# Kernel optimization log

Measured on AMD Instinct MI355X. Metric: run time of the kernel, lower is better.

The kernel has to match this reference:

```python
import jax, jax.numpy as jnp
import numpy as np

N_NODES = 100000
N_EDGES = 1600000
DIMS = [512, 200, 175, 125, 75, 50]


def setup_inputs() -> dict:
    key = jax.random.key(0)
    ks = jax.random.split(key, 12)
    inp = {
        "x": jax.random.normal(ks[0], (N_NODES, DIMS[0]), dtype=jnp.float32),
        "edge_index": jax.random.randint(ks[1], (2, N_EDGES), 0, N_NODES, dtype=jnp.int32),
    }
    for i in range(5):
        fan_in, fan_out = DIMS[i], DIMS[i + 1]
        scale = 1.0 / np.sqrt(fan_in)
        inp[f"W{i+1}"] = jax.random.uniform(ks[2 + 2 * i], (fan_in, fan_out), minval=-scale, maxval=scale, dtype=jnp.float32)
        inp[f"b{i+1}"] = jnp.zeros((fan_out,), dtype=jnp.float32)
    return inp


def _gcn_norm(edge_index, n_nodes):
    # add self loops, then symmetric normalization D^-1/2 (A+I) D^-1/2
    loop = jnp.arange(n_nodes, dtype=edge_index.dtype)
    src = jnp.concatenate([edge_index[0], loop])
    dst = jnp.concatenate([edge_index[1], loop])
    deg = jax.ops.segment_sum(jnp.ones_like(dst, dtype=jnp.float32), dst, num_segments=n_nodes)
    dinv = jnp.where(deg > 0, jax.lax.rsqrt(deg), 0.0)
    norm = dinv[src] * dinv[dst]  # [E+N]
    return src, dst, norm


def _gcn_layer(x, W, b, src, dst, norm, n_nodes):
    h = x @ W                                   # [N, out] dense GEMM
    msg = h[src] * norm[:, None]                # gather + scale  [E+N, out]
    agg = jax.ops.segment_sum(msg, dst, num_segments=n_nodes)  # scatter-add
    return agg + b


def reference(x, edge_index, W1, b1, W2, b2, W3, b3, W4, b4, W5, b5):
    n = x.shape[0]
    src, dst, norm = _gcn_norm(edge_index, n)
    h = jax.nn.relu(_gcn_layer(x, W1, b1, src, dst, norm, n))
    h = jax.nn.relu(_gcn_layer(h, W2, b2, src, dst, norm, n))
    h = jax.nn.relu(_gcn_layer(h, W3, b3, src, dst, norm, n))
    h = jax.nn.relu(_gcn_layer(h, W4, b4, src, dst, norm, n))
    return _gcn_layer(h, W5, b5, src, dst, norm, n)
```

## Files before the change

kernel.cpp:

```cpp
#include <hip/hip_runtime.h>
#include <hip/hip_bf16.h>


typedef float f32x4 __attribute__((ext_vector_type(4)));
typedef short bf16x8 __attribute__((ext_vector_type(8)));
typedef ushort u16x4 __attribute__((ext_vector_type(4)));
typedef ushort u16x8 __attribute__((ext_vector_type(8)));

static const int GDIMS[6] = {512, 200, 175, 125, 75, 50};


__global__ void zero_kernel(int* __restrict__ p, int n) {
    int i = blockIdx.x * blockDim.x + threadIdx.x;
    for (; i < n; i += gridDim.x * blockDim.x) p[i] = 0;
}

__global__ void hist_kernel(const int* __restrict__ dst, int E, int* __restrict__ deg) {
    int i = blockIdx.x * blockDim.x + threadIdx.x;
    for (; i < E; i += gridDim.x * blockDim.x) atomicAdd(&deg[dst[i]], 1);
}

__global__ __launch_bounds__(1024) void scan_kernel(const int* __restrict__ deg,
                                                    int* __restrict__ rowptr, int N) {
    __shared__ int sums[1024];
    int t = threadIdx.x;
    int chunk = (N + 1023) >> 10;
    int lo = t * chunk;
    int hi = lo + chunk; if (hi > N) hi = N;
    if (lo > N) lo = N;
    int s = 0;
    for (int i = lo; i < hi; ++i) s += deg[i];
    sums[t] = s;
    __syncthreads();
    for (int off = 1; off < 1024; off <<= 1) {
        int v = (t >= off) ? sums[t - off] : 0;
        __syncthreads();
        sums[t] += v;
        __syncthreads();
    }
    int run = (t > 0) ? sums[t - 1] : 0;
    for (int i = lo; i < hi; ++i) { rowptr[i] = run; run += deg[i]; }
    if (t == 1023) rowptr[N] = run;
}

__global__ void dinv_kernel(const int* __restrict__ deg, float* __restrict__ dinv, int N) {
    int i = blockIdx.x * blockDim.x + threadIdx.x;
    for (; i < N; i += gridDim.x * blockDim.x)
        dinv[i] = rsqrtf((float)(deg[i] + 1));
}

__global__ void copy_kernel(const int* __restrict__ a, int* __restrict__ b, int n) {
    int i = blockIdx.x * blockDim.x + threadIdx.x;
    for (; i < n; i += gridDim.x * blockDim.x) b[i] = a[i];
}

__global__ void scatter_kernel(const int* __restrict__ src, const int* __restrict__ dst,
                               int E, int* __restrict__ cursor, int* __restrict__ csrc) {
    int i = blockIdx.x * blockDim.x + threadIdx.x;
    for (; i < E; i += gridDim.x * blockDim.x) {
        int d = dst[i];
        int pos = atomicAdd(&cursor[d], 1);
        csrc[pos] = src[i];
    }
}


__global__ void wsplit_kernel(const float* __restrict__ W, int K, int Nout,
                              int Kp, ushort* __restrict__ Whi, ushort* __restrict__ Wlo) {
    int k = blockIdx.x * blockDim.x + threadIdx.x;
    int n = blockIdx.y;
    if (k >= Kp) return;
    float v = (k < K && n < Nout) ? W[(size_t)k * Nout + n] : 0.f;
    __bf16 h = (__bf16)v;
    ushort hb = __builtin_bit_cast(ushort, h);
    float hf = __builtin_bit_cast(float, (unsigned)hb << 16);
    __bf16 l = (__bf16)(v - hf);
    Whi[(size_t)n * Kp + k] = hb;
    Wlo[(size_t)n * Kp + k] = __builtin_bit_cast(ushort, l);
}


__device__ inline f32x4 mfma16(bf16x8 a, bf16x8 b, f32x4 c) {
    return __builtin_amdgcn_mfma_f32_16x16x32_bf16(a, b, c, 0, 0, 0);
}

__device__ inline void split8(f32x4 a0, f32x4 a1, u16x8& hi, u16x8& lo) {
    float af[8] = {a0[0], a0[1], a0[2], a0[3], a1[0], a1[1], a1[2], a1[3]};
#pragma unroll
    for (int e = 0; e < 8; ++e) {
        __bf16 h = (__bf16)af[e];
        ushort hb = __builtin_bit_cast(ushort, h);
        float hf = __builtin_bit_cast(float, (unsigned)hb << 16);
        __bf16 l = (__bf16)(af[e] - hf);
        hi[e] = hb;
        lo[e] = __builtin_bit_cast(ushort, l);
    }
}


template<int WM, int WN>
__global__ __launch_bounds__(WM * WN * 64) void gemm_t(
    const float* __restrict__ A, int lda, int Arows,
    const ushort* __restrict__ Bhi, const ushort* __restrict__ Blo, int Kp,
    const float* __restrict__ dinv, int N,
    float* __restrict__ C, int ldc)
{
    constexpr int BM = WM * 64;
    constexpr int T = WM * WN * 64;
    constexpr int SROW = BM + 2;
    __shared__ ushort Ah[4 * SROW * 8];
    __shared__ ushort Al[4 * SROW * 8];

    const int tid = threadIdx.x;
    const int lane = tid & 63;
    const int wave = tid >> 6;
    const int wm = (WM == 1) ? 0 : (wave % WM);
    const int wn = (WM == 1) ? wave : (wave / WM);
    const int m0 = blockIdx.x * BM;
    const int kg = lane >> 4;
    const int l16 = lane & 15;

    const ushort* bp[4];
#pragma unroll
    for (int fn = 0; fn < 4; ++fn) {
        int n = wn * 64 + fn * 16 + l16;
        bp[fn] = Bhi + (size_t)n * Kp + kg * 8;
    }
    const size_t lo_off = (size_t)(Blo - Bhi);

    f32x4 acc[4][4];
#pragma unroll
    for (int i = 0; i < 4; ++i)
#pragma unroll
        for (int j = 0; j < 4; ++j) acc[i][j] = (f32x4)0.f;

    for (int k0 = 0; k0 < Kp; k0 += 32) {
        for (int j = tid; j < BM * 4; j += T) {
            int row = j >> 2, jk = j & 3;
            int gr = m0 + row; if (gr > Arows - 1) gr = Arows - 1;
            const float* ap = A + (size_t)gr * lda + k0 + jk * 8;
            f32x4 a0 = *(const f32x4*)ap;
            f32x4 a1 = *(const f32x4*)(ap + 4);
            u16x8 hi, lo;
            split8(a0, a1, hi, lo);
            int idx = (jk * SROW + row) * 8;
            *(u16x8*)&Ah[idx] = hi;
            *(u16x8*)&Al[idx] = lo;
        }
        __syncthreads();
        bf16x8 bh[4], bl[4], ah[4], al[4];
#pragma unroll
        for (int fn = 0; fn < 4; ++fn) {
            bh[fn] = *(const bf16x8*)(bp[fn] + k0);
            bl[fn] = *(const bf16x8*)(bp[fn] + lo_off + k0);
        }
#pragma unroll
        for (int fm = 0; fm < 4; ++fm) {
            int idx = (kg * SROW + wm * 64 + fm * 16 + l16) * 8;
            ah[fm] = *(const bf16x8*)&Ah[idx];
            al[fm] = *(const bf16x8*)&Al[idx];
        }
#pragma unroll
        for (int fm = 0; fm < 4; ++fm)
#pragma unroll
            for (int fn = 0; fn < 4; ++fn) {
                acc[fm][fn] = mfma16(ah[fm], bh[fn], acc[fm][fn]);
                acc[fm][fn] = mfma16(ah[fm], bl[fn], acc[fm][fn]);
                acc[fm][fn] = mfma16(al[fm], bh[fn], acc[fm][fn]);
            }
        __syncthreads();
    }

#pragma unroll
    for (int fm = 0; fm < 4; ++fm)
#pragma unroll
        for (int fn = 0; fn < 4; ++fn) {
            int col = wn * 64 + fn * 16 + l16;
            if (col < ldc) {
#pragma unroll
                for (int r = 0; r < 4; ++r) {
                    int row = m0 + wm * 64 + fm * 16 + kg * 4 + r;
                    float dv = (row < N) ? dinv[row] : 0.f;
                    C[(size_t)row * ldc + col] = acc[fm][fn][r] * dv;
                }
            }
        }
}


template<int WM, int WN>
__global__ __launch_bounds__(WM * WN * 64) void gemm_ps(
    const ushort* __restrict__ Ahi, const ushort* __restrict__ Alo, int lda, int Arows,
    const ushort* __restrict__ Bhi, const ushort* __restrict__ Blo, int Kp,
    const float* __restrict__ dinv, int N,
    float* __restrict__ C, int ldc)
{
    constexpr int BM = WM * 64;
    constexpr int T = WM * WN * 64;
    constexpr int SROW = BM + 2;
    __shared__ ushort Ah[4 * SROW * 8];
    __shared__ ushort Al[4 * SROW * 8];

    const int tid = threadIdx.x;
    const int lane = tid & 63;
    const int wave = tid >> 6;
    const int wm = (WM == 1) ? 0 : (wave % WM);
    const int wn = (WM == 1) ? wave : (wave / WM);
    const int m0 = blockIdx.x * BM;
    const int kg = lane >> 4;
    const int l16 = lane & 15;

    const size_t alo = (size_t)(Alo - Ahi);
    const ushort* bp[4];
#pragma unroll
    for (int fn = 0; fn < 4; ++fn) {
        int n = wn * 64 + fn * 16 + l16;
        bp[fn] = Bhi + (size_t)n * Kp + kg * 8;
    }
    const size_t blo = (size_t)(Blo - Bhi);

    f32x4 acc[4][4];
#pragma unroll
    for (int i = 0; i < 4; ++i)
#pragma unroll
        for (int j = 0; j < 4; ++j) acc[i][j] = (f32x4)0.f;

    for (int k0 = 0; k0 < Kp; k0 += 32) {
        for (int j = tid; j < BM * 4; j += T) {
            int row = j >> 2, jk = j & 3;
            int gr = m0 + row; if (gr > Arows - 1) gr = Arows - 1;
            const ushort* s = Ahi + (size_t)gr * lda + k0 + jk * 8;
            int idx = (jk * SROW + row) * 8;
            *(u16x8*)&Ah[idx] = *(const u16x8*)s;
            *(u16x8*)&Al[idx] = *(const u16x8*)(s + alo);
        }
        __syncthreads();
        bf16x8 bh[4], bl[4], ah[4], al[4];
#pragma unroll
        for (int fn = 0; fn < 4; ++fn) {
            bh[fn] = *(const bf16x8*)(bp[fn] + k0);
            bl[fn] = *(const bf16x8*)(bp[fn] + blo + k0);
        }
#pragma unroll
        for (int fm = 0; fm < 4; ++fm) {
            int idx = (kg * SROW + wm * 64 + fm * 16 + l16) * 8;
            ah[fm] = *(const bf16x8*)&Ah[idx];
            al[fm] = *(const bf16x8*)&Al[idx];
        }
#pragma unroll
        for (int fm = 0; fm < 4; ++fm)
#pragma unroll
            for (int fn = 0; fn < 4; ++fn) {
                acc[fm][fn] = mfma16(ah[fm], bh[fn], acc[fm][fn]);
                acc[fm][fn] = mfma16(ah[fm], bl[fn], acc[fm][fn]);
                acc[fm][fn] = mfma16(al[fm], bh[fn], acc[fm][fn]);
            }
        __syncthreads();
    }

#pragma unroll
    for (int fm = 0; fm < 4; ++fm)
#pragma unroll
        for (int fn = 0; fn < 4; ++fn) {
            int col = wn * 64 + fn * 16 + l16;
            if (col < ldc) {
#pragma unroll
                for (int r = 0; r < 4; ++r) {
                    int row = m0 + wm * 64 + fm * 16 + kg * 4 + r;
                    float dv = (row < N) ? dinv[row] : 0.f;
                    C[(size_t)row * ldc + col] = acc[fm][fn][r] * dv;
                }
            }
        }
}


template<int ND4T, bool FIN>
__global__ __launch_bounds__(256) void agg_t(
    const float* __restrict__ g, int ld4,
    const int* __restrict__ rowptr, const int* __restrict__ csrc,
    const float* __restrict__ dinv, const float* __restrict__ bias,
    int D, int N,
    ushort* __restrict__ Ahi, ushort* __restrict__ Alo, int ldo,
    float* __restrict__ outF, int ldof)
{
    unsigned gt = blockIdx.x * 256u + threadIdx.x;
    unsigned node = gt / (unsigned)ND4T;
    unsigned f4 = gt - node * (unsigned)ND4T;
    if (node >= (unsigned)N) return;

    const f32x4* g4 = (const f32x4*)g;
    const unsigned l4 = (unsigned)ld4;

    f32x4 a0 = g4[(size_t)node * l4 + f4];
    f32x4 a1 = (f32x4)0.f, a2 = (f32x4)0.f, a3 = (f32x4)0.f;
    int beg = rowptr[node], end = rowptr[node + 1];
    int j = beg;
    for (; j + 3 < end; j += 4) {
        unsigned s0 = csrc[j], s1 = csrc[j + 1], s2 = csrc[j + 2], s3 = csrc[j + 3];
        a0 += g4[(size_t)s0 * l4 + f4];
        a1 += g4[(size_t)s1 * l4 + f4];
        a2 += g4[(size_t)s2 * l4 + f4];
        a3 += g4[(size_t)s3 * l4 + f4];
    }
    for (; j < end; ++j) a0 += g4[(size_t)csrc[j] * l4 + f4];

    f32x4 s = (a0 + a1) + (a2 + a3);
    float di = dinv[node];

    if (FIN) {
#pragma unroll
        for (int e = 0; e < 4; ++e) {
            int f = (int)f4 * 4 + e;
            if (f < D) outF[(size_t)node * ldof + f] = fmaf(di, s[e], bias[f]);
        }
    } else {
        u16x4 hv, lv;
#pragma unroll
        for (int e = 0; e < 4; ++e) {
            int f = (int)f4 * 4 + e;
            float val = 0.f;
            if (f < D) val = fmaxf(fmaf(di, s[e], bias[f]), 0.f);
            __bf16 h = (__bf16)val;
            ushort hb = __builtin_bit_cast(ushort, h);
            float hf = __builtin_bit_cast(float, (unsigned)hb << 16);
            __bf16 l = (__bf16)(val - hf);
            hv[e] = hb;
            lv[e] = __builtin_bit_cast(ushort, l);
        }
        *(u16x4*)(Ahi + (size_t)node * ldo + f4 * 4) = hv;
        *(u16x4*)(Alo + (size_t)node * ldo + f4 * 4) = lv;
    }
}


extern "C" void kernel_launch(void* const* d_in, const int* in_sizes, int n_in,
                              void* d_out, int out_size, void* d_ws, size_t ws_size,
                              hipStream_t stream) {
    const float* x = (const float*)d_in[0];
    const int* ei = (const int*)d_in[1];
    int E = in_sizes[1] / 2;
    int N = in_sizes[0] / GDIMS[0];
    int Mp = ((N + 255) / 256) * 256;
    const int* src = ei;
    const int* dst = ei + E;

    const float* W[5];
    const float* bia[5];
    for (int i = 0; i < 5; ++i) {
        W[i] = (const float*)d_in[2 + 2 * i];
        bia[i] = (const float*)d_in[3 + 2 * i];
    }

    char* ws = (char*)d_ws;
    size_t off = 0;
    auto alloc = [&](size_t bytes) -> void* {
        void* p = ws + off;
        off += (bytes + 255) & ~(size_t)255;
        return p;
    };
    int* deg = (int*)alloc((size_t)N * 4);
    int* rowptr = (int*)alloc((size_t)(N + 1) * 4);
    int* cursor = (int*)alloc((size_t)N * 4);
    float* dinv = (float*)alloc((size_t)N * 4);
    int* csrc = (int*)alloc((size_t)E * 4);
    float* g = (float*)alloc((size_t)Mp * 224 * 4);
    ushort* Ahi = (ushort*)alloc((size_t)Mp * 224 * 2);
    ushort* Alo = (ushort*)alloc((size_t)Mp * 224 * 2);
    ushort* Whi[5];
    ushort* Wlo[5];
    int NB[5] = {256, 192, 128, 128, 64};
    int KP[5] = {512, 224, 192, 128, 96};
    for (int l = 0; l < 5; ++l) {
        Whi[l] = (ushort*)alloc((size_t)NB[l] * KP[l] * 2);
        Wlo[l] = (ushort*)alloc((size_t)NB[l] * KP[l] * 2);
    }
    (void)ws_size;

    zero_kernel<<<1024, 256, 0, stream>>>(deg, N);
    hist_kernel<<<2048, 256, 0, stream>>>(dst, E, deg);
    scan_kernel<<<1, 1024, 0, stream>>>(deg, rowptr, N);
    dinv_kernel<<<512, 256, 0, stream>>>(deg, dinv, N);
    copy_kernel<<<512, 256, 0, stream>>>(rowptr, cursor, N);
    scatter_kernel<<<2048, 256, 0, stream>>>(src, dst, E, cursor, csrc);

    for (int l = 0; l < 5; ++l) {
        dim3 gw((KP[l] + 255) / 256, NB[l]);
        wsplit_kernel<<<gw, 256, 0, stream>>>(W[l], GDIMS[l], GDIMS[l + 1], KP[l],
                                              Whi[l], Wlo[l]);
    }

    auto aggBlocks = [&](int nd4t) { return (unsigned)(((size_t)N * nd4t + 255) / 256); };

    gemm_t<1, 4><<<Mp / 64, 256, 0, stream>>>(x, 512, N, Whi[0], Wlo[0], 512,
                                              dinv, N, g, 224);
    agg_t<56, false><<<aggBlocks(56), 256, 0, stream>>>(g, 56, rowptr, csrc, dinv,
                                                        bia[0], 200, N, Ahi, Alo, 224,
                                                        nullptr, 0);
    gemm_ps<1, 3><<<Mp / 64, 192, 0, stream>>>(Ahi, Alo, 224, N, Whi[1], Wlo[1], 224,
                                               dinv, N, g, 192);
    agg_t<48, false><<<aggBlocks(48), 256, 0, stream>>>(g, 48, rowptr, csrc, dinv,
                                                        bia[1], 175, N, Ahi, Alo, 192,
                                                        nullptr, 0);
    gemm_ps<2, 2><<<Mp / 128, 256, 0, stream>>>(Ahi, Alo, 192, N, Whi[2], Wlo[2], 192,
                                                dinv, N, g, 128);
    agg_t<32, false><<<aggBlocks(32), 256, 0, stream>>>(g, 32, rowptr, csrc, dinv,
                                                        bia[2], 125, N, Ahi, Alo, 128,
                                                        nullptr, 0);
    gemm_ps<2, 2><<<Mp / 128, 256, 0, stream>>>(Ahi, Alo, 128, N, Whi[3], Wlo[3], 128,
                                                dinv, N, g, 96);
    agg_t<24, false><<<aggBlocks(24), 256, 0, stream>>>(g, 24, rowptr, csrc, dinv,
                                                        bia[3], 75, N, Ahi, Alo, 96,
                                                        nullptr, 0);
    gemm_ps<4, 1><<<Mp / 256, 256, 0, stream>>>(Ahi, Alo, 96, N, Whi[4], Wlo[4], 96,
                                                dinv, N, g, 64);
    agg_t<13, true><<<aggBlocks(13), 256, 0, stream>>>(g, 16, rowptr, csrc, dinv,
                                                       bia[4], 50, N, nullptr, nullptr, 0,
                                                       (float*)d_out, 50);
    (void)out_size; (void)n_in;
}
```

Baseline: 1.376 ms.

## Pre-swizzle activations and weights into MFMA fragment layout, drop LDS staging

The aggregation kernels now write the bf16 hi/lo activations straight into a blocked layout that matches the 16x16x32 MFMA fragments. The weight-splitting kernel writes the weights for layers 2-5 in the same layout. The new GEMM then loads A and B fragments directly from global memory, with no shared-memory staging and no barriers. Aggregation also switches to a power-of-two number of lanes per node, which leaves some lanes idle and stops writing zeros to the padded feature columns, so those columns may keep stale data.

```diff
diff --git a/kernel.cpp b/kernel.cpp
--- a/kernel.cpp
+++ b/kernel.cpp
@@ -79,6 +79,24 @@
     Wlo[(size_t)n * Kp + k] = __builtin_bit_cast(ushort, l);
 }
 
+__global__ void wsplit_sw(const float* __restrict__ W, int K, int Nout,
+                          int Kp, ushort* __restrict__ Whi, ushort* __restrict__ Wlo) {
+    int k = blockIdx.x * blockDim.x + threadIdx.x;
+    int n = blockIdx.y;
+    if (k >= Kp) return;
+    int KQ = Kp >> 3;
+    float v = (k < K && n < Nout) ? W[(size_t)k * Nout + n] : 0.f;
+    __bf16 h = (__bf16)v;
+    ushort hb = __builtin_bit_cast(ushort, h);
+    float hf = __builtin_bit_cast(float, (unsigned)hb << 16);
+    __bf16 l = (__bf16)(v - hf);
+    int mb = n >> 6, fm = (n >> 4) & 3, l16 = n & 15;
+    int kq = k >> 3, ko = k & 7;
+    size_t idx = ((((size_t)mb * KQ + kq) * 4 + fm) * 16 + l16) * 8 + ko;
+    Whi[idx] = hb;
+    Wlo[idx] = __builtin_bit_cast(ushort, l);
+}
+
 
 __device__ inline f32x4 mfma16(bf16x8 a, bf16x8 b, f32x4 c) {
     return __builtin_amdgcn_mfma_f32_16x16x32_bf16(a, b, c, 0, 0, 0);
@@ -188,36 +206,30 @@
 }
 
 
-template<int WM, int WN>
-__global__ __launch_bounds__(WM * WN * 64) void gemm_ps(
-    const ushort* __restrict__ Ahi, const ushort* __restrict__ Alo, int lda, int Arows,
-    const ushort* __restrict__ Bhi, const ushort* __restrict__ Blo, int Kp,
+template<int WN>
+__global__ __launch_bounds__(WN * 64) void gemm_sw(
+    const ushort* __restrict__ Ahi, const ushort* __restrict__ Alo, int KQ, int Kp,
+    const ushort* __restrict__ Bhi, const ushort* __restrict__ Blo,
     const float* __restrict__ dinv, int N,
     float* __restrict__ C, int ldc)
 {
-    constexpr int BM = WM * 64;
-    constexpr int T = WM * WN * 64;
-    constexpr int SROW = BM + 2;
-    __shared__ ushort Ah[4 * SROW * 8];
-    __shared__ ushort Al[4 * SROW * 8];
-
-    const int tid = threadIdx.x;
-    const int lane = tid & 63;
-    const int wave = tid >> 6;
-    const int wm = (WM == 1) ? 0 : (wave % WM);
-    const int wn = (WM == 1) ? wave : (wave / WM);
-    const int m0 = blockIdx.x * BM;
+    const int lane = threadIdx.x & 63;
+    const int wn = threadIdx.x >> 6;
+    const int m0 = blockIdx.x * 64;
+    const int mb = m0 >> 6;
     const int kg = lane >> 4;
     const int l16 = lane & 15;
 
     const size_t alo = (size_t)(Alo - Ahi);
+    const size_t blo = (size_t)(Blo - Bhi);
+    const ushort* ap[4];
     const ushort* bp[4];
 #pragma unroll
-    for (int fn = 0; fn < 4; ++fn) {
-        int n = wn * 64 + fn * 16 + l16;
-        bp[fn] = Bhi + (size_t)n * Kp + kg * 8;
-    }
-    const size_t blo = (size_t)(Blo - Bhi);
+    for (int fm = 0; fm < 4; ++fm)
+        ap[fm] = Ahi + ((((size_t)mb * KQ + kg) * 4 + fm) * 16 + l16) * 8;
+#pragma unroll
+    for (int fn = 0; fn < 4; ++fn)
+        bp[fn] = Bhi + ((((size_t)wn * KQ + kg) * 4 + fn) * 16 + l16) * 8;
 
     f32x4 acc[4][4];
 #pragma unroll
@@ -225,27 +237,19 @@
 #pragma unroll
         for (int j = 0; j < 4; ++j) acc[i][j] = (f32x4)0.f;
 
-    for (int k0 = 0; k0 < Kp; k0 += 32) {
-        for (int j = tid; j < BM * 4; j += T) {
-            int row = j >> 2, jk = j & 3;
-            int gr = m0 + row; if (gr > Arows - 1) gr = Arows - 1;
-            const ushort* s = Ahi + (size_t)gr * lda + k0 + jk * 8;
-            int idx = (jk * SROW + row) * 8;
-            *(u16x8*)&Ah[idx] = *(const u16x8*)s;
-            *(u16x8*)&Al[idx] = *(const u16x8*)(s + alo);
-        }
-        __syncthreads();
-        bf16x8 bh[4], bl[4], ah[4], al[4];
+    const int nsteps = Kp >> 5;
+    for (int t = 0; t < nsteps; ++t) {
+        const size_t off = (size_t)t * 2048;
+        bf16x8 ah[4], al4[4], bh[4], bl[4];
+#pragma unroll
+        for (int fm = 0; fm < 4; ++fm) {
+            ah[fm] = *(const bf16x8*)(ap[fm] + off);
+            al4[fm] = *(const bf16x8*)(ap[fm] + alo + off);
+        }
 #pragma unroll
         for (int fn = 0; fn < 4; ++fn) {
-            bh[fn] = *(const bf16x8*)(bp[fn] + k0);
-            bl[fn] = *(const bf16x8*)(bp[fn] + blo + k0);
-        }
-#pragma unroll
-        for (int fm = 0; fm < 4; ++fm) {
-            int idx = (kg * SROW + wm * 64 + fm * 16 + l16) * 8;
-            ah[fm] = *(const bf16x8*)&Ah[idx];
-            al[fm] = *(const bf16x8*)&Al[idx];
+            bh[fn] = *(const bf16x8*)(bp[fn] + off);
+            bl[fn] = *(const bf16x8*)(bp[fn] + blo + off);
         }
 #pragma unroll
         for (int fm = 0; fm < 4; ++fm)
@@ -253,9 +257,8 @@
             for (int fn = 0; fn < 4; ++fn) {
                 acc[fm][fn] = mfma16(ah[fm], bh[fn], acc[fm][fn]);
                 acc[fm][fn] = mfma16(ah[fm], bl[fn], acc[fm][fn]);
-                acc[fm][fn] = mfma16(al[fm], bh[fn], acc[fm][fn]);
+                acc[fm][fn] = mfma16(al4[fm], bh[fn], acc[fm][fn]);
             }
-        __syncthreads();
     }
 
 #pragma unroll
@@ -266,7 +269,7 @@
             if (col < ldc) {
 #pragma unroll
                 for (int r = 0; r < 4; ++r) {
-                    int row = m0 + wm * 64 + fm * 16 + kg * 4 + r;
+                    int row = m0 + fm * 16 + kg * 4 + r;
                     float dv = (row < N) ? dinv[row] : 0.f;
                     C[(size_t)row * ldc + col] = acc[fm][fn][r] * dv;
                 }
@@ -275,50 +278,49 @@
 }
 
 
-template<int ND4T, bool FIN>
-__global__ __launch_bounds__(256) void agg_t(
-    const float* __restrict__ g, int ld4,
+template<int L>
+__global__ __launch_bounds__(256) void agg_sw(
+    const float* __restrict__ g, int ldg, int nd4,
     const int* __restrict__ rowptr, const int* __restrict__ csrc,
     const float* __restrict__ dinv, const float* __restrict__ bias,
     int D, int N,
-    ushort* __restrict__ Ahi, ushort* __restrict__ Alo, int ldo,
-    float* __restrict__ outF, int ldof)
+    ushort* __restrict__ Ahi, ushort* __restrict__ Alo, int KQ,
+    float* __restrict__ outF, int ldof, int fin)
 {
-    unsigned gt = blockIdx.x * 256u + threadIdx.x;
-    unsigned node = gt / (unsigned)ND4T;
-    unsigned f4 = gt - node * (unsigned)ND4T;
-    if (node >= (unsigned)N) return;
+    int node = blockIdx.x * (256 / L) + threadIdx.x / L;
+    if (node >= N) return;
+    int f4 = threadIdx.x & (L - 1);
+    if (f4 >= nd4) return;
 
     const f32x4* g4 = (const f32x4*)g;
-    const unsigned l4 = (unsigned)ld4;
-
-    f32x4 a0 = g4[(size_t)node * l4 + f4];
+    int ld4 = ldg >> 2;
+    f32x4 a0 = g4[(size_t)node * ld4 + f4];
     f32x4 a1 = (f32x4)0.f, a2 = (f32x4)0.f, a3 = (f32x4)0.f;
     int beg = rowptr[node], end = rowptr[node + 1];
     int j = beg;
     for (; j + 3 < end; j += 4) {
-        unsigned s0 = csrc[j], s1 = csrc[j + 1], s2 = csrc[j + 2], s3 = csrc[j + 3];
-        a0 += g4[(size_t)s0 * l4 + f4];
-        a1 += g4[(size_t)s1 * l4 + f4];
-        a2 += g4[(size_t)s2 * l4 + f4];
-        a3 += g4[(size_t)s3 * l4 + f4];
-    }
-    for (; j < end; ++j) a0 += g4[(size_t)csrc[j] * l4 + f4];
+        int s0 = csrc[j], s1 = csrc[j + 1], s2 = csrc[j + 2], s3 = csrc[j + 3];
+        a0 += g4[(size_t)s0 * ld4 + f4];
+        a1 += g4[(size_t)s1 * ld4 + f4];
+        a2 += g4[(size_t)s2 * ld4 + f4];
+        a3 += g4[(size_t)s3 * ld4 + f4];
+    }
+    for (; j < end; ++j) a0 += g4[(size_t)csrc[j] * ld4 + f4];
 
     f32x4 s = (a0 + a1) + (a2 + a3);
     float di = dinv[node];
 
-    if (FIN) {
+    if (fin) {
 #pragma unroll
         for (int e = 0; e < 4; ++e) {
-            int f = (int)f4 * 4 + e;
+            int f = f4 * 4 + e;
             if (f < D) outF[(size_t)node * ldof + f] = fmaf(di, s[e], bias[f]);
         }
     } else {
         u16x4 hv, lv;
 #pragma unroll
         for (int e = 0; e < 4; ++e) {
-            int f = (int)f4 * 4 + e;
+            int f = f4 * 4 + e;
             float val = 0.f;
             if (f < D) val = fmaxf(fmaf(di, s[e], bias[f]), 0.f);
             __bf16 h = (__bf16)val;
@@ -328,8 +330,11 @@
             hv[e] = hb;
             lv[e] = __builtin_bit_cast(ushort, l);
         }
-        *(u16x4*)(Ahi + (size_t)node * ldo + f4 * 4) = hv;
-        *(u16x4*)(Alo + (size_t)node * ldo + f4 * 4) = lv;
+        int mb = node >> 6, fm = (node >> 4) & 3, l16 = node & 15;
+        int kq = f4 >> 1, ko = (f4 & 1) * 4;
+        size_t idx = ((((size_t)mb * KQ + kq) * 4 + fm) * 16 + l16) * 8 + ko;
+        *(u16x4*)(Ahi + idx) = hv;
+        *(u16x4*)(Alo + idx) = lv;
     }
 }
 
@@ -384,38 +389,41 @@
     copy_kernel<<<512, 256, 0, stream>>>(rowptr, cursor, N);
     scatter_kernel<<<2048, 256, 0, stream>>>(src, dst, E, cursor, csrc);
 
-    for (int l = 0; l < 5; ++l) {
+    {
+        dim3 gw((KP[0] + 255) / 256, NB[0]);
+        wsplit_kernel<<<gw, 256, 0, stream>>>(W[0], GDIMS[0], GDIMS[1], KP[0],
+                                              Whi[0], Wlo[0]);
+    }
+    for (int l = 1; l < 5; ++l) {
         dim3 gw((KP[l] + 255) / 256, NB[l]);
-        wsplit_kernel<<<gw, 256, 0, stream>>>(W[l], GDIMS[l], GDIMS[l + 1], KP[l],
-                                              Whi[l], Wlo[l]);
-    }
-
-    auto aggBlocks = [&](int nd4t) { return (unsigned)(((size_t)N * nd4t + 255) / 256); };
+        wsplit_sw<<<gw, 256, 0, stream>>>(W[l], GDIMS[l], GDIMS[l + 1], KP[l],
+                                          Whi[l], Wlo[l]);
+    }
 
     gemm_t<1, 4><<<Mp / 64, 256, 0, stream>>>(x, 512, N, Whi[0], Wlo[0], 512,
                                               dinv, N, g, 224);
-    agg_t<56, false><<<aggBlocks(56), 256, 0, stream>>>(g, 56, rowptr, csrc, dinv,
-                                                        bia[0], 200, N, Ahi, Alo, 224,
-                                                        nullptr, 0);
-    gemm_ps<1, 3><<<Mp / 64, 192, 0, stream>>>(Ahi, Alo, 224, N, Whi[1], Wlo[1], 224,
-                                               dinv, N, g, 192);
-    agg_t<48, false><<<aggBlocks(48), 256, 0, stream>>>(g, 48, rowptr, csrc, dinv,
-                                                        bia[1], 175, N, Ahi, Alo, 192,
-                                                        nullptr, 0);
-    gemm_ps<2, 2><<<Mp / 128, 256, 0, stream>>>(Ahi, Alo, 192, N, Whi[2], Wlo[2], 192,
-                                                dinv, N, g, 128);
-    agg_t<32, false><<<aggBlocks(32), 256, 0, stream>>>(g, 32, rowptr, csrc, dinv,
-                                                        bia[2], 125, N, Ahi, Alo, 128,
-                                                        nullptr, 0);
-    gemm_ps<2, 2><<<Mp / 128, 256, 0, stream>>>(Ahi, Alo, 128, N, Whi[3], Wlo[3], 128,
-                                                dinv, N, g, 96);
-    agg_t<24, false><<<aggBlocks(24), 256, 0, stream>>>(g, 24, rowptr, csrc, dinv,
-                                                        bia[3], 75, N, Ahi, Alo, 96,
-                                                        nullptr, 0);
-    gemm_ps<4, 1><<<Mp / 256, 256, 0, stream>>>(Ahi, Alo, 96, N, Whi[4], Wlo[4], 96,
-                                                dinv, N, g, 64);
-    agg_t<13, true><<<aggBlocks(13), 256, 0, stream>>>(g, 16, rowptr, csrc, dinv,
-                                                       bia[4], 50, N, nullptr, nullptr, 0,
-                                                       (float*)d_out, 50);
+    agg_sw<64><<<(N + 3) / 4, 256, 0, stream>>>(g, 224, 50, rowptr, csrc, dinv,
+                                                bia[0], 200, N, Ahi, Alo, 28,
+                                                nullptr, 0, 0);
+    gemm_sw<3><<<Mp / 64, 192, 0, stream>>>(Ahi, Alo, 28, 224, Whi[1], Wlo[1],
+                                            dinv, N, g, 192);
+    agg_sw<64><<<(N + 3) / 4, 256, 0, stream>>>(g, 192, 44, rowptr, csrc, dinv,
+                                                bia[1], 175, N, Ahi, Alo, 24,
+                                                nullptr, 0, 0);
+    gemm_sw<2><<<Mp / 64, 128, 0, stream>>>(Ahi, Alo, 24, 192, Whi[2], Wlo[2],
+                                            dinv, N, g, 128);
+    agg_sw<32><<<(N + 7) / 8, 256, 0, stream>>>(g, 128, 32, rowptr, csrc, dinv,
+                                                bia[2], 125, N, Ahi, Alo, 16,
+                                                nullptr, 0, 0);
+    gemm_sw<2><<<Mp / 64, 128, 0, stream>>>(Ahi, Alo, 16, 128, Whi[3], Wlo[3],
+                                            dinv, N, g, 96);
+    agg_sw<32><<<(N + 7) / 8, 256, 0, stream>>>(g, 96, 19, rowptr, csrc, dinv,
+                                                bia[3], 75, N, Ahi, Alo, 12,
+                                                nullptr, 0, 0);
+    gemm_sw<1><<<Mp / 64, 64, 0, stream>>>(Ahi, Alo, 12, 96, Whi[4], Wlo[4],
+                                           dinv, N, g, 64);
+    agg_sw<16><<<(N + 15) / 16, 256, 0, stream>>>(g, 64, 13, rowptr, csrc, dinv,
+                                                  bia[4], 50, N, nullptr, nullptr, 0,
+                                                  (float*)d_out, 50, 1);
     (void)out_size; (void)n_in;
 }
```

After: 1.354 ms. Within noise of the previous version (-1.5%).
